# Performance work log

Hardware: AMD Instinct MI355X
Metric: run time of the kernel (lower is better)

Reference implementation:

```python
import jax, jax.numpy as jnp
import numpy as np

NUM_IDS = 64  # static upper bound on track ids (0 = background)


def setup_inputs() -> dict:
    key = jax.random.key(0)
    k1, k2 = jax.random.split(key)
    B, F, C, H, W = 4, 8, 16, 256, 256
    embeddings = jax.random.normal(k1, (B, F, C, H, W), dtype=jnp.float32)
    track_ids = jax.random.randint(k2, (B, F, 1, H, W), 0, NUM_IDS, dtype=jnp.int32)
    return {"embeddings": embeddings, "track_ids": track_ids}


def reference(embeddings, track_ids):
    B, F, C, H, W = embeddings.shape
    K = NUM_IDS
    ids = track_ids[:, :, 0]  # (B, F, H, W)
    # global segment id: one bucket per (b, f, track_id)
    seg = ((jnp.arange(B * F, dtype=jnp.int32).reshape(B, F, 1, 1)) * K + ids).reshape(-1)
    data = jnp.transpose(embeddings, (0, 1, 3, 4, 2)).reshape(-1, C)  # (B*F*H*W, C)
    sums = jax.ops.segment_sum(data, seg, num_segments=B * F * K).reshape(B, F, K, C)
    counts = jax.ops.segment_sum(jnp.ones((B * F * H * W,), embeddings.dtype), seg,
                                 num_segments=B * F * K).reshape(B, F, K)
    means = sums / jnp.maximum(counts, 1)[..., None]  # (B, F, K, C)
    present = counts > 0
    # id must be > 0 (background excluded) and present in both consecutive frames
    pair_valid = present[:, :-1] & present[:, 1:] & (jnp.arange(K) > 0)  # (B, F-1, K)
    dist = jnp.sum((means[:, :-1] - means[:, 1:]) ** 2, axis=-1)  # (B, F-1, K)
    total = jnp.sum(jnp.where(pair_valid, dist, jnp.zeros_like(dist)))
    n_valid = jnp.sum(pair_valid).astype(embeddings.dtype)
    return jnp.where(n_valid > 0, total / n_valid, jnp.zeros_like(total))
```

## Files before the change

kernel.cpp:

```cpp
#include <hip/hip_runtime.h>
#include <hip/hip_bf16.h>

#define NB 4
#define NF 8
#define NC 16
#define NK 64
#define HW 65536
#define NBF 32
#define BPF 64
#define PPB (HW / BPF)
#define PPW (PPB / 4)
#define STEPS (PPW / 32)

typedef __attribute__((ext_vector_type(8))) short bf16x8;
typedef __attribute__((ext_vector_type(4))) float f32x4;

__global__ __launch_bounds__(256) void zero_kernel(float* __restrict__ p, int n) {
    int i = blockIdx.x * blockDim.x + threadIdx.x;
    if (i < n) p[i] = 0.0f;
}

__device__ __forceinline__ short f32_to_bf16_bits(float x) {
    union { float f; unsigned u; } v; v.f = x;
    unsigned r = v.u + 0x7FFFu + ((v.u >> 16) & 1u);
    return (short)(r >> 16);
}

__global__ __launch_bounds__(256) void accum_mfma(const float* __restrict__ E,
                                                  const int* __restrict__ T,
                                                  float* __restrict__ gsum,
                                                  float* __restrict__ gcnt) {
    const int tid = threadIdx.x;
    const int wv  = tid >> 6;
    const int l   = tid & 63;
    const int col = l & 15;
    const int grp = l >> 4;

    const int bf    = blockIdx.x / BPF;
    const int chunk = blockIdx.x % BPF;
    const int base  = chunk * PPB + wv * PPW + grp * 8;

    const int*   Tp = T + (size_t)bf * HW + base;
    const float* Ep = E + ((size_t)bf * NC + col) * HW + base;

    f32x4 accS[4], accC[4];
    #pragma unroll
    for (int t = 0; t < 4; ++t) { accS[t] = (f32x4){0,0,0,0}; accC[t] = (f32x4){0,0,0,0}; }

    bf16x8 bOnes;
    {
        const short ov = (col == 0) ? (short)0x3F80 : (short)0;
        #pragma unroll
        for (int j = 0; j < 8; ++j) bOnes[j] = ov;
    }

    for (int s = 0; s < STEPS; ++s) {
        const int off = s * 32;
        const int4   i0 = *reinterpret_cast<const int4*>(Tp + off);
        const int4   i1 = *reinterpret_cast<const int4*>(Tp + off + 4);
        const float4 d0 = *reinterpret_cast<const float4*>(Ep + off);
        const float4 d1 = *reinterpret_cast<const float4*>(Ep + off + 4);

        const int   idv[8] = {i0.x, i0.y, i0.z, i0.w, i1.x, i1.y, i1.z, i1.w};
        const float dv[8]  = {d0.x, d0.y, d0.z, d0.w, d1.x, d1.y, d1.z, d1.w};

        bf16x8 bF;
        #pragma unroll
        for (int j = 0; j < 8; ++j) bF[j] = f32_to_bf16_bits(dv[j]);

        #pragma unroll
        for (int t = 0; t < 4; ++t) {
            const int ktar = t * 16 + col;
            bf16x8 aT;
            #pragma unroll
            for (int j = 0; j < 8; ++j) aT[j] = (idv[j] == ktar) ? (short)0x3F80 : (short)0;
            accS[t] = __builtin_amdgcn_mfma_f32_16x16x32_bf16(aT, bF,    accS[t], 0, 0, 0);
            accC[t] = __builtin_amdgcn_mfma_f32_16x16x32_bf16(aT, bOnes, accC[t], 0, 0, 0);
        }
    }

    __shared__ float lsum[4][NK][NC];
    __shared__ float lcnt[4][NK];
    #pragma unroll
    for (int t = 0; t < 4; ++t) {
        #pragma unroll
        for (int j = 0; j < 4; ++j) {
            const int k = t * 16 + grp * 4 + j;
            lsum[wv][k][col] = accS[t][j];
            if (col == 0) lcnt[wv][k] = accC[t][j];
        }
    }
    __syncthreads();

    float* gs = gsum + (size_t)bf * NK * NC;
    const float* lp = &lsum[0][0][0];
    for (int i = tid; i < NK * NC; i += 256) {
        atomicAdd(&gs[i], lp[i] + lp[NK*NC + i] + lp[2*NK*NC + i] + lp[3*NK*NC + i]);
    }
    if (tid < NK) {
        atomicAdd(&gcnt[(size_t)bf * NK + tid],
                  lcnt[0][tid] + lcnt[1][tid] + lcnt[2][tid] + lcnt[3][tid]);
    }
}

__global__ __launch_bounds__(256) void finish_kernel(const float* __restrict__ gsum,
                                                     const float* __restrict__ gcnt,
                                                     float* __restrict__ out) {
    float total = 0.0f, nv = 0.0f;
    for (int idx = threadIdx.x; idx < NB * (NF - 1) * NK; idx += 256) {
        const int k = idx & 63;
        const int bfr = idx >> 6;
        const int b = bfr / (NF - 1);
        const int f = bfr % (NF - 1);
        const int bf0 = b * NF + f;
        if (k == 0) continue;
        const float c0 = gcnt[bf0 * NK + k];
        const float c1 = gcnt[(bf0 + 1) * NK + k];
        if (c0 > 0.0f && c1 > 0.0f) {
            const float r0 = 1.0f / c0, r1 = 1.0f / c1;
            float d = 0.0f;
            #pragma unroll
            for (int c = 0; c < NC; ++c) {
                const float m0 = gsum[(size_t)bf0 * (NK * NC) + k * NC + c] * r0;
                const float m1 = gsum[(size_t)(bf0 + 1) * (NK * NC) + k * NC + c] * r1;
                const float df = m0 - m1;
                d += df * df;
            }
            total += d;
            nv += 1.0f;
        }
    }
    const int lane = threadIdx.x & 63;
    const int wvi  = threadIdx.x >> 6;
    #pragma unroll
    for (int off = 32; off > 0; off >>= 1) {
        total += __shfl_down(total, off, 64);
        nv    += __shfl_down(nv, off, 64);
    }
    __shared__ float sT[4], sN[4];
    if (lane == 0) { sT[wvi] = total; sN[wvi] = nv; }
    __syncthreads();
    if (threadIdx.x == 0) {
        const float t = sT[0] + sT[1] + sT[2] + sT[3];
        const float n = sN[0] + sN[1] + sN[2] + sN[3];
        out[0] = (n > 0.0f) ? (t / n) : 0.0f;
    }
}

extern "C" void kernel_launch(void* const* d_in, const int* in_sizes, int n_in,
                              void* d_out, int out_size, void* d_ws, size_t ws_size,
                              hipStream_t stream) {
    const float* E = (const float*)d_in[0];
    const int*   T = (const int*)d_in[1];
    float* out = (float*)d_out;

    float* gsum = (float*)d_ws;
    float* gcnt = gsum + NBF * NK * NC;
    const int ntot = NBF * NK * NC + NBF * NK;

    zero_kernel<<<(ntot + 255) / 256, 256, 0, stream>>>(gsum, ntot);
    accum_mfma<<<NBF * BPF, 256, 0, stream>>>(E, T, gsum, gcnt);
    finish_kernel<<<1, 256, 0, stream>>>(gsum, gcnt, out);
}
```

Before: 213.9 us.

## Replace global atomics with per-block partials and separate reduce kernel; stage ids in LDS

```diff
diff --git a/kernel.cpp b/kernel.cpp
--- a/kernel.cpp
+++ b/kernel.cpp
@@ -11,14 +11,10 @@
 #define PPB (HW / BPF)
 #define PPW (PPB / 4)
 #define STEPS (PPW / 32)
+#define PARTSZ 1088
 
 typedef __attribute__((ext_vector_type(8))) short bf16x8;
 typedef __attribute__((ext_vector_type(4))) float f32x4;
-
-__global__ __launch_bounds__(256) void zero_kernel(float* __restrict__ p, int n) {
-    int i = blockIdx.x * blockDim.x + threadIdx.x;
-    if (i < n) p[i] = 0.0f;
-}
 
 __device__ __forceinline__ short f32_to_bf16_bits(float x) {
     union { float f; unsigned u; } v; v.f = x;
@@ -28,8 +24,11 @@
 
 __global__ __launch_bounds__(256) void accum_mfma(const float* __restrict__ E,
                                                   const int* __restrict__ T,
-                                                  float* __restrict__ gsum,
-                                                  float* __restrict__ gcnt) {
+                                                  float* __restrict__ part) {
+    __shared__ int   sids[PPB];
+    __shared__ float lsum[4][NK][NC];
+    __shared__ float lcnt[4][NK];
+
     const int tid = threadIdx.x;
     const int wv  = tid >> 6;
     const int l   = tid & 63;
@@ -38,10 +37,14 @@
 
     const int bf    = blockIdx.x / BPF;
     const int chunk = blockIdx.x % BPF;
-    const int base  = chunk * PPB + wv * PPW + grp * 8;
 
-    const int*   Tp = T + (size_t)bf * HW + base;
+    *reinterpret_cast<int4*>(&sids[tid * 4]) =
+        *reinterpret_cast<const int4*>(T + (size_t)bf * HW + chunk * PPB + tid * 4);
+    __syncthreads();
+
+    const int base = chunk * PPB + wv * PPW + grp * 8;
     const float* Ep = E + ((size_t)bf * NC + col) * HW + base;
+    const int* sip = &sids[wv * PPW + grp * 8];
 
     f32x4 accS[4], accC[4];
     #pragma unroll
@@ -54,10 +57,11 @@
         for (int j = 0; j < 8; ++j) bOnes[j] = ov;
     }
 
+    #pragma unroll 2
     for (int s = 0; s < STEPS; ++s) {
         const int off = s * 32;
-        const int4   i0 = *reinterpret_cast<const int4*>(Tp + off);
-        const int4   i1 = *reinterpret_cast<const int4*>(Tp + off + 4);
+        const int4   i0 = *reinterpret_cast<const int4*>(sip + off);
+        const int4   i1 = *reinterpret_cast<const int4*>(sip + off + 4);
         const float4 d0 = *reinterpret_cast<const float4*>(Ep + off);
         const float4 d1 = *reinterpret_cast<const float4*>(Ep + off + 4);
 
@@ -79,8 +83,6 @@
         }
     }
 
-    __shared__ float lsum[4][NK][NC];
-    __shared__ float lcnt[4][NK];
     #pragma unroll
     for (int t = 0; t < 4; ++t) {
         #pragma unroll
@@ -92,14 +94,37 @@
     }
     __syncthreads();
 
-    float* gs = gsum + (size_t)bf * NK * NC;
+    float* pp = part + (size_t)blockIdx.x * PARTSZ;
     const float* lp = &lsum[0][0][0];
     for (int i = tid; i < NK * NC; i += 256) {
-        atomicAdd(&gs[i], lp[i] + lp[NK*NC + i] + lp[2*NK*NC + i] + lp[3*NK*NC + i]);
+        pp[i] = lp[i] + lp[NK*NC + i] + lp[2*NK*NC + i] + lp[3*NK*NC + i];
     }
     if (tid < NK) {
-        atomicAdd(&gcnt[(size_t)bf * NK + tid],
-                  lcnt[0][tid] + lcnt[1][tid] + lcnt[2][tid] + lcnt[3][tid]);
+        pp[NK * NC + tid] = lcnt[0][tid] + lcnt[1][tid] + lcnt[2][tid] + lcnt[3][tid];
+    }
+}
+
+__global__ __launch_bounds__(256) void reduce_kernel(const float* __restrict__ part,
+                                                     float* __restrict__ gsum,
+                                                     float* __restrict__ gcnt) {
+    const int e = blockIdx.x * 256 + threadIdx.x;
+    if (e < NBF * NK * NC) {
+        const int bf = e >> 10;
+        const int i  = e & 1023;
+        const float* p = part + (size_t)(bf * BPF) * PARTSZ + i;
+        float s = 0.0f;
+        #pragma unroll 8
+        for (int blk = 0; blk < BPF; ++blk) s += p[(size_t)blk * PARTSZ];
+        gsum[e] = s;
+    } else {
+        const int e2 = e - NBF * NK * NC;
+        const int bf = e2 >> 6;
+        const int k  = e2 & 63;
+        const float* p = part + (size_t)(bf * BPF) * PARTSZ + NK * NC + k;
+        float s = 0.0f;
+        #pragma unroll 8
+        for (int blk = 0; blk < BPF; ++blk) s += p[(size_t)blk * PARTSZ];
+        gcnt[e2] = s;
     }
 }
 
@@ -154,11 +179,11 @@
     const int*   T = (const int*)d_in[1];
     float* out = (float*)d_out;
 
-    float* gsum = (float*)d_ws;
+    float* part = (float*)d_ws;
+    float* gsum = part + (size_t)(NBF * BPF) * PARTSZ;
     float* gcnt = gsum + NBF * NK * NC;
-    const int ntot = NBF * NK * NC + NBF * NK;
 
-    zero_kernel<<<(ntot + 255) / 256, 256, 0, stream>>>(gsum, ntot);
-    accum_mfma<<<NBF * BPF, 256, 0, stream>>>(E, T, gsum, gcnt);
+    accum_mfma<<<NBF * BPF, 256, 0, stream>>>(E, T, part);
+    reduce_kernel<<<(NBF * NK * NC + NBF * NK) / 256, 256, 0, stream>>>(part, gsum, gcnt);
     finish_kernel<<<1, 256, 0, stream>>>(gsum, gcnt, out);
 }
```

Measured after the change: 213.6 us. About the same (-0.1%).
